# Performance work log

Measured on AMD Instinct MI355X. Metric: run time of the kernel, lower is better.

## Reference

```python
import jax, jax.numpy as jnp
import numpy as np
from jax import lax

V, E, HD, T = 32000, 256, 256, 4   # vocab, embed dim, lstm hidden (bidir total), tagset (BMES)
H = HD // 2                        # hidden per direction
B, S = 64, 1024


def setup_inputs() -> dict:
    key = jax.random.key(0)
    ks = jax.random.split(key, 16)
    sc = 0.1
    return {
        "sentences": jax.random.randint(ks[0], (B, S), 0, V, dtype=jnp.int32),
        "embed": jax.random.normal(ks[1], (V, E), jnp.float32) * sc,
        "w_ih_f": jax.random.normal(ks[2], (4 * H, E), jnp.float32) * sc,
        "w_hh_f": jax.random.normal(ks[3], (4 * H, H), jnp.float32) * sc,
        "b_ih_f": jax.random.normal(ks[4], (4 * H,), jnp.float32) * sc,
        "b_hh_f": jax.random.normal(ks[5], (4 * H,), jnp.float32) * sc,
        "w_ih_r": jax.random.normal(ks[6], (4 * H, E), jnp.float32) * sc,
        "w_hh_r": jax.random.normal(ks[7], (4 * H, H), jnp.float32) * sc,
        "b_ih_r": jax.random.normal(ks[8], (4 * H,), jnp.float32) * sc,
        "b_hh_r": jax.random.normal(ks[9], (4 * H,), jnp.float32) * sc,
        "w_out": jax.random.normal(ks[10], (T, HD), jnp.float32) * sc,
        "b_out": jax.random.normal(ks[11], (T,), jnp.float32) * sc,
        "start_t": jax.random.normal(ks[12], (T,), jnp.float32) * sc,
        "end_t": jax.random.normal(ks[13], (T,), jnp.float32) * sc,
        "trans": jax.random.normal(ks[14], (T, T), jnp.float32) * sc,
    }


def _lstm_pass(x, w_ih, w_hh, b_ih, b_hh):
    # x: [S, B, E]; PyTorch gate order i, f, g, o; zero initial state.
    bsz = x.shape[1]
    hdim = w_hh.shape[1]
    b = b_ih + b_hh

    def step(carry, xt):
        h, c = carry
        z = xt @ w_ih.T + h @ w_hh.T + b  # [B, 4H]
        i, f, g, o = jnp.split(z, 4, axis=-1)
        c = jax.nn.sigmoid(f) * c + jax.nn.sigmoid(i) * jnp.tanh(g)
        h = jax.nn.sigmoid(o) * jnp.tanh(c)
        return (h, c), h

    init = (jnp.zeros((bsz, hdim), x.dtype), jnp.zeros((bsz, hdim), x.dtype))
    _, hs = lax.scan(step, init, x)
    return hs  # [S, B, H]


def _emissions(sentences, embed, w_ih_f, w_hh_f, b_ih_f, b_hh_f,
               w_ih_r, w_hh_r, b_ih_r, b_hh_r, w_out, b_out):
    x = embed[sentences]                # [B, S, E]
    xs = jnp.transpose(x, (1, 0, 2))    # [S, B, E]
    hf = _lstm_pass(xs, w_ih_f, w_hh_f, b_ih_f, b_hh_f)
    hr = _lstm_pass(xs[::-1], w_ih_r, w_hh_r, b_ih_r, b_hh_r)[::-1]
    h = jnp.concatenate([hf, hr], axis=-1)        # [S, B, 2H]
    return h @ w_out.T + b_out                    # [S, B, T] emissions


def _viterbi_decode(feats, start_t, end_t, trans):
    # feats: [S, B, T] (no mask: all sequences full length, matching crf.decode on dense batch)
    score0 = start_t + feats[0]  # [B, T]

    def fwd_step(score, emit):
        nxt = score[:, :, None] + trans[None, :, :] + emit[:, None, :]  # [B, Tprev, Tcur]
        return jnp.max(nxt, axis=1), jnp.argmax(nxt, axis=1)

    final, bps = lax.scan(fwd_step, score0, feats[1:])  # bps: [S-1, B, T]
    final = final + end_t
    last = jnp.argmax(final, axis=1)  # [B]

    def back_step(tag, bp):
        prev = jnp.take_along_axis(bp, tag[:, None], axis=1)[:, 0]
        return prev, prev

    _, path_head = lax.scan(back_step, last, bps, reverse=True)  # [S-1, B], tags at t=0..S-2
    path = jnp.concatenate([path_head, last[None]], axis=0)      # [S, B]
    return jnp.transpose(path, (1, 0)).astype(jnp.int32)         # [B, S]


def reference(sentences, embed, w_ih_f, w_hh_f, b_ih_f, b_hh_f,
              w_ih_r, w_hh_r, b_ih_r, b_hh_r, w_out, b_out,
              start_t, end_t, trans):
    feats = _emissions(sentences, embed, w_ih_f, w_hh_f, b_ih_f, b_hh_f,
                       w_ih_r, w_hh_r, b_ih_r, b_hh_r, w_out, b_out)
    return _viterbi_decode(feats, start_t, end_t, trans)
```

## Files before the change

kernel.cpp:

```cpp
#include <hip/hip_runtime.h>
#include <cstdint>
#include <cstddef>

#define SLEN 1024
#define BATCH 64
#define EDIM 256
#define HDIM 128
#define GDIM 512
#define NTAG 4
#define VOCAB 32000

typedef float f2 __attribute__((ext_vector_type(2)));
typedef float f4 __attribute__((ext_vector_type(4)));


__device__ __forceinline__ float sigm_f(float x) {
    return 1.0f / (1.0f + __expf(-x));
}
__device__ __forceinline__ float tanh_f(float x) {
    return 1.0f - 2.0f / (1.0f + __expf(2.0f * x));
}

template <int CTRL>
__device__ __forceinline__ float quad_perm(float x) {
    return __int_as_float(
        __builtin_amdgcn_mov_dpp(__float_as_int(x), CTRL, 0xF, 0xF, true));
}
#define QP_XOR1 0xB1
#define QP_XOR2 0x4E
#define QP_MIR8 0x141
#define QP_BC0  0x00
#define QP_BC1  0x55
#define QP_BC2  0xAA
#define QP_BC3  0xFF

__global__ __launch_bounds__(512) void table_k(
    const float* __restrict__ embed,
    const float* __restrict__ w_ih_f, const float* __restrict__ w_ih_r,
    const float* __restrict__ b_ih_f, const float* __restrict__ b_hh_f,
    const float* __restrict__ b_ih_r, const float* __restrict__ b_hh_r,
    float* __restrict__ T)
{
    __shared__ __align__(16) float smem[12288];
    float* As = smem;
    const int t  = threadIdx.x;
    const int tm = t >> 8;
    const int tt = t & 255;
    float* Bs = smem + 4096 + tm * 4096;

    const int mt  = blockIdx.x;
    const int cp  = blockIdx.y;
    const int nt  = cp * 2 + tm;
    const int dir = nt >> 2;
    const float* W  = dir ? w_ih_r : w_ih_f;
    const float* bi = dir ? b_ih_r : b_ih_f;
    const float* bh = dir ? b_hh_r : b_hh_f;
    const int ncol = (nt & 3) * 128;
    const int r0   = mt * 128;

    const int sra = t & 127;
    const int qa  = t >> 7;
    const float* arow = embed + (size_t)(r0 + sra) * EDIM + qa * 8;

    const int srb = tt & 127;
    const int hb  = tt >> 7;
    const float* brow = W + (size_t)(ncol + srb) * EDIM + hb * 16;

    const int tx = tt & 15, ty = tt >> 4;

    f2 acc[8][4];
    #pragma unroll
    for (int i = 0; i < 8; ++i)
        #pragma unroll
        for (int jj = 0; jj < 4; ++jj) acc[i][jj] = (f2)(0.0f);

    for (int kt = 0; kt < 8; ++kt) {
        const int k0 = kt * 32;
        __syncthreads();
        {
            float4 v0 = *(const float4*)(arow + k0);
            float4 v1 = *(const float4*)(arow + k0 + 4);
            const int kk = qa * 8;
            As[(kk + 0) * 128 + sra] = v0.x;
            As[(kk + 1) * 128 + sra] = v0.y;
            As[(kk + 2) * 128 + sra] = v0.z;
            As[(kk + 3) * 128 + sra] = v0.w;
            As[(kk + 4) * 128 + sra] = v1.x;
            As[(kk + 5) * 128 + sra] = v1.y;
            As[(kk + 6) * 128 + sra] = v1.z;
            As[(kk + 7) * 128 + sra] = v1.w;
        }
        #pragma unroll
        for (int i = 0; i < 4; ++i) {
            float4 v = *(const float4*)(brow + k0 + i * 4);
            const int kk = hb * 16 + i * 4;
            Bs[(kk + 0) * 128 + srb] = v.x;
            Bs[(kk + 1) * 128 + srb] = v.y;
            Bs[(kk + 2) * 128 + srb] = v.z;
            Bs[(kk + 3) * 128 + srb] = v.w;
        }
        __syncthreads();

        #pragma unroll 8
        for (int k = 0; k < 32; ++k) {
            const f4 a0  = *(const f4*)&As[k * 128 + ty * 4];
            const f4 a1  = *(const f4*)&As[k * 128 + 64 + ty * 4];
            const f4 bq0 = *(const f4*)&Bs[k * 128 + tx * 4];
            const f4 bq1 = *(const f4*)&Bs[k * 128 + 64 + tx * 4];
            float av[8] = {a0.x, a0.y, a0.z, a0.w, a1.x, a1.y, a1.z, a1.w};
            f2 bv[4];
            bv[0] = __builtin_shufflevector(bq0, bq0, 0, 1);
            bv[1] = __builtin_shufflevector(bq0, bq0, 2, 3);
            bv[2] = __builtin_shufflevector(bq1, bq1, 0, 1);
            bv[3] = __builtin_shufflevector(bq1, bq1, 2, 3);
            #pragma unroll
            for (int i = 0; i < 8; ++i) {
                f2 as; as.x = av[i]; as.y = av[i];
                #pragma unroll
                for (int jj = 0; jj < 4; ++jj)
                    acc[i][jj] += as * bv[jj];
            }
        }
    }

    float bias0[4], bias1[4];
    #pragma unroll
    for (int j = 0; j < 4; ++j) {
        bias0[j] = bi[ncol + tx * 4 + j] + bh[ncol + tx * 4 + j];
        bias1[j] = bi[ncol + 64 + tx * 4 + j] + bh[ncol + 64 + tx * 4 + j];
    }

    #pragma unroll
    for (int i = 0; i < 8; ++i) {
        const int row = r0 + ((i < 4) ? (ty * 4 + i) : (64 + ty * 4 + i - 4));
        float* zp = T + (size_t)row * 1024 + dir * 512 + ncol;
        float4 o0, o1;
        o0.x = acc[i][0].x + bias0[0]; o0.y = acc[i][0].y + bias0[1];
        o0.z = acc[i][1].x + bias0[2]; o0.w = acc[i][1].y + bias0[3];
        o1.x = acc[i][2].x + bias1[0]; o1.y = acc[i][2].y + bias1[1];
        o1.z = acc[i][3].x + bias1[2]; o1.w = acc[i][3].y + bias1[3];
        *(float4*)(zp + tx * 4)      = o0;
        *(float4*)(zp + 64 + tx * 4) = o1;
    }
}

__global__ __launch_bounds__(512) __attribute__((amdgpu_waves_per_eu(2, 2)))
void lstm_k(
    const float* __restrict__ T, const int* __restrict__ sent,
    const float* __restrict__ w_hh_f, const float* __restrict__ w_hh_r,
    float* __restrict__ H)
{
    __shared__ __align__(16) float sh_h[320];
    __shared__ int sh_tok[SLEN];

    const int bid = blockIdx.x;
    const int b   = bid & 63;
    const int dir = bid >> 6;
    const int q   = threadIdx.x;
    const int p   = q & 7;
    const int Q   = q >> 3;
    const int gt  = p & 3;
    const int hi  = p >> 2;
    const int u   = Q + hi * 64;

    const float* Whh = dir ? w_hh_r : w_hh_f;

    f2 w2[8][8];
    #pragma unroll
    for (int pr = 0; pr < 8; ++pr) {
        const int uu = (pr & 4) ? (Q + 64) : Q;
        const int gg = pr & 3;
        const f2* src =
            (const f2*)(Whh + ((size_t)(gg * 128 + uu) * 128 + p * 16));
        #pragma unroll
        for (int i = 0; i < 8; ++i) w2[pr][i] = src[i];
    }
    #pragma unroll
    for (int pr = 0; pr < 8; ++pr)
        #pragma unroll
        for (int i = 0; i < 8; ++i)
            asm volatile("" : "+v"(w2[pr][i]));

    sh_tok[q]       = sent[b * SLEN + q];
    sh_tok[512 + q] = sent[b * SLEN + 512 + q];
    if (q < 128) sh_h[(q >> 5) * 36 + (q & 31)] = 0.0f;
    float c = 0.0f;
    __syncthreads();

    const int zcol = dir * 512 + gt * 128 + u;
    const ptrdiff_t hstride = dir ? -16384 : 16384;
    float* hg = H + ((size_t)(dir ? (SLEN - 1) : 0) * 64 + b) * 256
              + dir * 128 + u;

    const bool k4 = (p & 4) != 0;
    const bool k2 = (p & 2) != 0;
    const bool k1 = (p & 1) != 0;
    const float gsc  = (gt == 2) ? 2.0f : 1.0f;
    const float gofs = (gt == 2) ? -1.0f : 0.0f;
    const int shr = (p >> 1) * 36 + (p & 1) * 16;
    const int shw = (u >> 5) * 36 + (u & 31);

    float zcur[4], znxt[4];
    #pragma unroll
    for (int dt = 0; dt < 4; ++dt) {
        const int s = dir ? (SLEN - 1 - dt) : dt;
        zcur[dt] = T[((size_t)sh_tok[s] << 10) + zcol];
    }

    for (int t0 = 0; t0 < SLEN; t0 += 4) {
        const bool more = (t0 + 4 < SLEN);
        if (more) {
            #pragma unroll
            for (int dt = 0; dt < 4; ++dt) {
                const int tn = t0 + 4 + dt;
                const int s = dir ? (SLEN - 1 - tn) : tn;
                znxt[dt] = T[((size_t)sh_tok[s] << 10) + zcol];
            }
        }

        #pragma unroll
        for (int dt = 0; dt < 4; ++dt) {
            const f4* hp = (const f4*)(sh_h + (dt & 1) * 160 + shr);
            f2 hv[8];
            #pragma unroll
            for (int i = 0; i < 4; ++i) {
                f4 v = hp[i];
                hv[2 * i]     = __builtin_shufflevector(v, v, 0, 1);
                hv[2 * i + 1] = __builtin_shufflevector(v, v, 2, 3);
            }
            float s[8];
            #pragma unroll
            for (int pr = 0; pr < 8; ++pr) {
                f2 a = (f2)(0.0f);
                #pragma unroll
                for (int i = 0; i < 8; ++i) a += w2[pr][i] * hv[i];
                s[pr] = a.x + a.y;
            }
            float K1[4];
            #pragma unroll
            for (int j = 0; j < 4; ++j) {
                float keep = k4 ? s[j + 4] : s[j];
                float send = k4 ? s[j] : s[j + 4];
                K1[j] = keep + quad_perm<QP_MIR8>(send);
            }
            float K2[2];
            #pragma unroll
            for (int j = 0; j < 2; ++j) {
                float keep = k2 ? K1[j + 2] : K1[j];
                float send = k2 ? K1[j] : K1[j + 2];
                K2[j] = keep + quad_perm<QP_XOR2>(send);
            }
            float keep3 = k1 ? K2[1] : K2[0];
            float send3 = k1 ? K2[0] : K2[1];
            float zv = keep3 + quad_perm<QP_XOR1>(send3) + zcur[dt];

            float sgv = sigm_f(zv * gsc);
            float act = fmaf(sgv, gsc, gofs);

            float a_i = quad_perm<QP_BC0>(act);
            float a_f = quad_perm<QP_BC1>(act);
            float a_g = quad_perm<QP_BC2>(act);
            float a_o = quad_perm<QP_BC3>(act);
            c = a_f * c + a_i * a_g;
            float h = a_o * tanh_f(c);

            if (gt == 0) {
                sh_h[((dt + 1) & 1) * 160 + shw] = h;
                *hg = h;
            }
            hg += hstride;
            __syncthreads();
        }

        if (more) {
            #pragma unroll
            for (int dt = 0; dt < 4; ++dt) zcur[dt] = znxt[dt];
        }
    }
}

__device__ __forceinline__ void gemm_body(
    float* smem, int mt, int cp,
    const int* __restrict__ sent, const float* __restrict__ embed,
    const float* __restrict__ w_ih_f, const float* __restrict__ w_ih_r,
    const float* __restrict__ b_ih_f, const float* __restrict__ b_hh_f,
    const float* __restrict__ b_ih_r, const float* __restrict__ b_hh_r,
    float* __restrict__ Z, int base_f, int base_r)
{
    float* As = smem;
    const int t  = threadIdx.x;
    const int tm = t >> 8;
    const int tt = t & 255;
    float* Bs = smem + 4096 + tm * 4096;

    const int nt  = cp * 2 + tm;
    const int dir = nt >> 2;
    const float* W  = dir ? w_ih_r : w_ih_f;
    const float* bi = dir ? b_ih_r : b_ih_f;
    const float* bh = dir ? b_hh_r : b_hh_f;
    const int ncol = (nt & 3) * 128;
    const int r0   = mt * 128;

    const int sra = t & 127;
    const int qa  = t >> 7;
    const int r_loc = r0 + sra;
    const int s_loc = r_loc >> 6;
    const int b_    = r_loc & 63;
    const int s_glob = (dir ? base_r : base_f) + s_loc;
    const int tok = sent[b_ * SLEN + s_glob];
    const float* arow = embed + (size_t)tok * EDIM + qa * 8;

    const int srb = tt & 127;
    const int hb  = tt >> 7;
    const float* brow = W + (size_t)(ncol + srb) * EDIM + hb * 16;

    const int tx = tt & 15, ty = tt >> 4;

    f2 acc[8][4];
    #pragma unroll
    for (int i = 0; i < 8; ++i)
        #pragma unroll
        for (int jj = 0; jj < 4; ++jj) acc[i][jj] = (f2)(0.0f);

    for (int kt = 0; kt < 8; ++kt) {
        const int k0 = kt * 32;
        __syncthreads();
        {
            float4 v0 = *(const float4*)(arow + k0);
            float4 v1 = *(const float4*)(arow + k0 + 4);
            const int kk = qa * 8;
            As[(kk + 0) * 128 + sra] = v0.x;
            As[(kk + 1) * 128 + sra] = v0.y;
            As[(kk + 2) * 128 + sra] = v0.z;
            As[(kk + 3) * 128 + sra] = v0.w;
            As[(kk + 4) * 128 + sra] = v1.x;
            As[(kk + 5) * 128 + sra] = v1.y;
            As[(kk + 6) * 128 + sra] = v1.z;
            As[(kk + 7) * 128 + sra] = v1.w;
        }
        #pragma unroll
        for (int i = 0; i < 4; ++i) {
            float4 v = *(const float4*)(brow + k0 + i * 4);
            const int kk = hb * 16 + i * 4;
            Bs[(kk + 0) * 128 + srb] = v.x;
            Bs[(kk + 1) * 128 + srb] = v.y;
            Bs[(kk + 2) * 128 + srb] = v.z;
            Bs[(kk + 3) * 128 + srb] = v.w;
        }
        __syncthreads();

        #pragma unroll 8
        for (int k = 0; k < 32; ++k) {
            const f4 a0  = *(const f4*)&As[k * 128 + ty * 4];
            const f4 a1  = *(const f4*)&As[k * 128 + 64 + ty * 4];
            const f4 bq0 = *(const f4*)&Bs[k * 128 + tx * 4];
            const f4 bq1 = *(const f4*)&Bs[k * 128 + 64 + tx * 4];
            float av[8] = {a0.x, a0.y, a0.z, a0.w, a1.x, a1.y, a1.z, a1.w};
            f2 bv[4];
            bv[0] = __builtin_shufflevector(bq0, bq0, 0, 1);
            bv[1] = __builtin_shufflevector(bq0, bq0, 2, 3);
            bv[2] = __builtin_shufflevector(bq1, bq1, 0, 1);
            bv[3] = __builtin_shufflevector(bq1, bq1, 2, 3);
            #pragma unroll
            for (int i = 0; i < 8; ++i) {
                f2 as; as.x = av[i]; as.y = av[i];
                #pragma unroll
                for (int jj = 0; jj < 4; ++jj)
                    acc[i][jj] += as * bv[jj];
            }
        }
    }

    float bias0[4], bias1[4];
    #pragma unroll
    for (int j = 0; j < 4; ++j) {
        bias0[j] = bi[ncol + tx * 4 + j] + bh[ncol + tx * 4 + j];
        bias1[j] = bi[ncol + 64 + tx * 4 + j] + bh[ncol + 64 + tx * 4 + j];
    }

    #pragma unroll
    for (int i = 0; i < 8; ++i) {
        const int row = r0 + ((i < 4) ? (ty * 4 + i) : (64 + ty * 4 + i - 4));
        float* zp = Z + (size_t)row * 1024 + dir * 512 + ncol;
        float4 o0, o1;
        o0.x = acc[i][0].x + bias0[0]; o0.y = acc[i][0].y + bias0[1];
        o0.z = acc[i][1].x + bias0[2]; o0.w = acc[i][1].y + bias0[3];
        o1.x = acc[i][2].x + bias1[0]; o1.y = acc[i][2].y + bias1[1];
        o1.z = acc[i][3].x + bias1[2]; o1.w = acc[i][3].y + bias1[3];
        *(float4*)(zp + tx * 4)      = o0;
        *(float4*)(zp + 64 + tx * 4) = o1;
    }
}

__device__ __forceinline__ void lstm_body(
    float* smem,
    const float* __restrict__ Z, const float* __restrict__ w_hh_f,
    const float* __restrict__ w_hh_r, float* __restrict__ H,
    float* __restrict__ ST, int base_f, int base_r, int L, int first)
{
    float* sh_h = smem;

    const int bid = blockIdx.x;
    const int b   = bid & 63;
    const int dir = bid >> 6;
    const int q   = threadIdx.x;
    const int p   = q & 7;
    const int Q   = q >> 3;
    const int gt  = p & 3;
    const int hi  = p >> 2;
    const int u   = Q + hi * 64;

    const float* Whh = dir ? w_hh_r : w_hh_f;

    f2 w2[8][8];
    #pragma unroll
    for (int pr = 0; pr < 8; ++pr) {
        const int uu = (pr & 4) ? (Q + 64) : Q;
        const int gg = pr & 3;
        const f2* src =
            (const f2*)(Whh + ((size_t)(gg * 128 + uu) * 128 + p * 16));
        #pragma unroll
        for (int i = 0; i < 8; ++i) w2[pr][i] = src[i];
    }

    float* stp = ST + (size_t)(dir * 64 + b) * 256;
    if (q < 128)
        sh_h[(q >> 5) * 36 + (q & 31)] = first ? 0.0f : stp[q];
    float c = first ? 0.0f : stp[128 + u];

    const ptrdiff_t zstride = dir ? -65536 : 65536;
    const float* zp0 = Z + (size_t)b * 1024 + dir * 512
                     + (dir ? (size_t)(L - 1) * 65536 : 0) + gt * 128 + u;
    const ptrdiff_t hstride = dir ? -16384 : 16384;
    float* hg = H + ((size_t)(dir ? (base_r + L - 1) : base_f) * 64 + b) * 256
              + dir * 128 + u;

    const bool k4 = (p & 4) != 0;
    const bool k2 = (p & 2) != 0;
    const bool k1 = (p & 1) != 0;
    const float gsc  = (gt == 2) ? 2.0f : 1.0f;
    const float gofs = (gt == 2) ? -1.0f : 0.0f;
    const int shr = (p >> 1) * 36 + (p & 1) * 16;
    const int shw = (u >> 5) * 36 + (u & 31);

    float zcur[4], znxt[4];
    {
        const float* zp = zp0;
        #pragma unroll
        for (int dt = 0; dt < 4; ++dt) { zcur[dt] = *zp; zp += zstride; }
    }
    __syncthreads();

    float hlast = 0.0f;

    for (int t0 = 0; t0 < L; t0 += 4) {
        const bool more = (t0 + 4 < L);
        if (more) {
            const float* zp = zp0 + (ptrdiff_t)(t0 + 4) * zstride;
            #pragma unroll
            for (int dt = 0; dt < 4; ++dt) { znxt[dt] = *zp; zp += zstride; }
        }

        #pragma unroll
        for (int dt = 0; dt < 4; ++dt) {
            const f4* hp = (const f4*)(sh_h + (dt & 1) * 160 + shr);
            f2 hv[8];
            #pragma unroll
            for (int i = 0; i < 4; ++i) {
                f4 v = hp[i];
                hv[2 * i]     = __builtin_shufflevector(v, v, 0, 1);
                hv[2 * i + 1] = __builtin_shufflevector(v, v, 2, 3);
            }
            float s[8];
            #pragma unroll
            for (int pr = 0; pr < 8; ++pr) {
                f2 a = (f2)(0.0f);
                #pragma unroll
                for (int i = 0; i < 8; ++i) a += w2[pr][i] * hv[i];
                s[pr] = a.x + a.y;
            }
            float K1[4];
            #pragma unroll
            for (int j = 0; j < 4; ++j) {
                float keep = k4 ? s[j + 4] : s[j];
                float send = k4 ? s[j] : s[j + 4];
                K1[j] = keep + quad_perm<QP_MIR8>(send);
            }
            float K2[2];
            #pragma unroll
            for (int j = 0; j < 2; ++j) {
                float keep = k2 ? K1[j + 2] : K1[j];
                float send = k2 ? K1[j] : K1[j + 2];
                K2[j] = keep + quad_perm<QP_XOR2>(send);
            }
            float keep3 = k1 ? K2[1] : K2[0];
            float send3 = k1 ? K2[0] : K2[1];
            float zv = keep3 + quad_perm<QP_XOR1>(send3) + zcur[dt];

            float sgv = sigm_f(zv * gsc);
            float act = fmaf(sgv, gsc, gofs);

            float a_i = quad_perm<QP_BC0>(act);
            float a_f = quad_perm<QP_BC1>(act);
            float a_g = quad_perm<QP_BC2>(act);
            float a_o = quad_perm<QP_BC3>(act);
            c = a_f * c + a_i * a_g;
            float h = a_o * tanh_f(c);
            hlast = h;

            if (gt == 0) {
                sh_h[((dt + 1) & 1) * 160 + shw] = h;
                *hg = h;
            }
            hg += hstride;
            __syncthreads();
        }

        if (more) {
            #pragma unroll
            for (int dt = 0; dt < 4; ++dt) zcur[dt] = znxt[dt];
        }
    }

    if (gt == 0) {
        stp[u] = hlast;
        stp[128 + u] = c;
    }
}

__global__ __launch_bounds__(512) void fused_lstm_gemm(
    const int* __restrict__ sent, const float* __restrict__ embed,
    const float* __restrict__ w_ih_f, const float* __restrict__ w_ih_r,
    const float* __restrict__ b_ih_f, const float* __restrict__ b_hh_f,
    const float* __restrict__ b_ih_r, const float* __restrict__ b_hh_r,
    float* __restrict__ Zw, int gbase_f, int gbase_r, int mtiles,
    const float* __restrict__ Zr, const float* __restrict__ w_hh_f,
    const float* __restrict__ w_hh_r, float* __restrict__ H,
    float* __restrict__ ST, int lbase_f, int lbase_r, int L, int first)
{
    __shared__ __align__(16) float smem[12288];

    if (blockIdx.x < 128) {
        lstm_body(smem, Zr, w_hh_f, w_hh_r, H, ST, lbase_f, lbase_r, L, first);
    } else {
        const int g  = blockIdx.x - 128;
        const int mt = g % mtiles;
        const int cp = g / mtiles;
        gemm_body(smem, mt, cp, sent, embed, w_ih_f, w_ih_r,
                  b_ih_f, b_hh_f, b_ih_r, b_hh_r, Zw, gbase_f, gbase_r);
    }
}

__global__ __launch_bounds__(512) void gemm_zin(
    const int* __restrict__ sent, const float* __restrict__ embed,
    const float* __restrict__ w_ih_f, const float* __restrict__ w_ih_r,
    const float* __restrict__ b_ih_f, const float* __restrict__ b_hh_f,
    const float* __restrict__ b_ih_r, const float* __restrict__ b_hh_r,
    float* __restrict__ Z, int base_f, int base_r)
{
    __shared__ __align__(16) float smem[12288];
    gemm_body(smem, blockIdx.x, blockIdx.y, sent, embed, w_ih_f, w_ih_r,
              b_ih_f, b_hh_f, b_ih_r, b_hh_r, Z, base_f, base_r);
}

__global__ __launch_bounds__(256) void emissions_k(
    const float* __restrict__ H, const float* __restrict__ w_out,
    const float* __restrict__ b_out, float* __restrict__ F)
{
    const int gid = blockIdx.x * 256 + threadIdx.x;
    const int r   = gid >> 2;
    const int tg  = gid & 3;
    const float4* h4 = (const float4*)(H + (size_t)r * 256);
    const float4* w4 = (const float4*)(w_out + (size_t)tg * 256);
    float a0 = 0.f, a1 = 0.f, a2 = 0.f, a3 = 0.f;
    #pragma unroll 8
    for (int k = 0; k < 64; ++k) {
        float4 h = h4[k], w = w4[k];
        a0 = fmaf(h.x, w.x, a0); a1 = fmaf(h.y, w.y, a1);
        a2 = fmaf(h.z, w.z, a2); a3 = fmaf(h.w, w.w, a3);
    }
    F[gid] = ((a0 + a1) + (a2 + a3)) + b_out[tg];
}

__device__ __forceinline__ unsigned compose_map(unsigned a, unsigned b) {
    unsigned r = 0;
    #pragma unroll
    for (int jj = 0; jj < 4; ++jj) {
        unsigned bj = (b >> (jj * 8)) & 3u;
        unsigned aj = (a >> (bj * 8)) & 3u;
        r |= aj << (jj * 8);
    }
    return r;
}

__global__ __launch_bounds__(64) void viterbi_k(
    const float* __restrict__ F, const float* __restrict__ start_t,
    const float* __restrict__ end_t, const float* __restrict__ trans,
    int* __restrict__ out)
{
    const int b    = blockIdx.x;
    const int lane = threadIdx.x;
    __shared__ __align__(16) float sfeat[SLEN][NTAG];
    __shared__ unsigned sbp[SLEN];

    #pragma unroll
    for (int i = 0; i < 16; ++i) {
        int s = i * 64 + lane;
        ((float4*)sfeat)[s] = *(const float4*)(F + ((size_t)s * BATCH + b) * NTAG);
    }
    __syncthreads();

    const int cur = lane & 3;
    float tr0 = trans[0 * 4 + cur], tr1 = trans[1 * 4 + cur];
    float tr2 = trans[2 * 4 + cur], tr3 = trans[3 * 4 + cur];
    float sc = start_t[cur] + sfeat[0][cur];

    for (int s = 1; s < SLEN; ++s) {
        float ft = sfeat[s][cur];
        float s0 = __shfl(sc, 0), s1 = __shfl(sc, 1);
        float s2 = __shfl(sc, 2), s3 = __shfl(sc, 3);
        float c0 = s0 + tr0, c1 = s1 + tr1, c2 = s2 + tr2, c3 = s3 + tr3;
        float best = c0; int arg = 0;
        if (c1 > best) { best = c1; arg = 1; }
        if (c2 > best) { best = c2; arg = 2; }
        if (c3 > best) { best = c3; arg = 3; }
        sc = best + ft;
        unsigned bp = (unsigned)arg;
        unsigned b0 = __shfl(bp, 0), b1 = __shfl(bp, 1);
        unsigned b2 = __shfl(bp, 2), b3 = __shfl(bp, 3);
        if (lane == 0) sbp[s] = b0 | (b1 << 8) | (b2 << 16) | (b3 << 24);
    }
    sc += end_t[cur];
    float f0 = __shfl(sc, 0), f1 = __shfl(sc, 1);
    float f2v = __shfl(sc, 2), f3 = __shfl(sc, 3);
    int last = 0; float bb = f0;
    if (f1 > bb)  { bb = f1;  last = 1; }
    if (f2v > bb) { bb = f2v; last = 2; }
    if (f3 > bb)  { bb = f3;  last = 3; }
    __syncthreads();

    unsigned m[16];
    #pragma unroll
    for (int k = 0; k < 16; ++k) {
        int s = lane * 16 + k;
        m[k] = (s >= 1) ? sbp[s] : 0x03020100u;
    }
    unsigned G = m[15];
    #pragma unroll
    for (int k = 14; k >= 0; --k) G = compose_map(m[k], G);
    unsigned R = G;
    #pragma unroll
    for (int d = 1; d < 64; d <<= 1) {
        unsigned oo = __shfl_down(R, d);
        if (lane + d < 64) R = compose_map(R, oo);
    }
    unsigned P = __shfl_down(R, 1);
    if (lane == 63) P = 0x03020100u;

    int tcur = (int)((P >> (last * 8)) & 3u);
    int* ob = out + b * SLEN + lane * 16;
    ob[15] = tcur;
    #pragma unroll
    for (int k = 15; k >= 1; --k) {
        tcur = (int)((m[k] >> (tcur * 8)) & 3u);
        ob[k - 1] = tcur;
    }
}

extern "C" void kernel_launch(void* const* d_in, const int* in_sizes, int n_in,
                              void* d_out, int out_size, void* d_ws, size_t ws_size,
                              hipStream_t stream)
{
    const int*   sent    = (const int*)d_in[0];
    const float* embed   = (const float*)d_in[1];
    const float* w_ih_f  = (const float*)d_in[2];
    const float* w_hh_f  = (const float*)d_in[3];
    const float* b_ih_f  = (const float*)d_in[4];
    const float* b_hh_f  = (const float*)d_in[5];
    const float* w_ih_r  = (const float*)d_in[6];
    const float* w_hh_r  = (const float*)d_in[7];
    const float* b_ih_r  = (const float*)d_in[8];
    const float* b_hh_r  = (const float*)d_in[9];
    const float* w_out   = (const float*)d_in[10];
    const float* b_out   = (const float*)d_in[11];
    const float* start_t = (const float*)d_in[12];
    const float* end_t   = (const float*)d_in[13];
    const float* trans   = (const float*)d_in[14];
    int* out = (int*)d_out;

    const size_t H_FLOATS  = (size_t)SLEN * BATCH * 256;
    const size_t F_FLOATS  = (size_t)SLEN * BATCH * NTAG;
    const size_t T_FLOATS  = (size_t)VOCAB * 1024;
    const size_t ST_FLOATS = (size_t)2 * BATCH * 256;

    const size_t table_need = (T_FLOATS + H_FLOATS + F_FLOATS) * sizeof(float);

    if (ws_size >= table_need) {
        float* T = (float*)d_ws;
        float* H = T + T_FLOATS;
        float* F = H + H_FLOATS;

        table_k<<<dim3(250, 4), 512, 0, stream>>>(
            embed, w_ih_f, w_ih_r, b_ih_f, b_hh_f, b_ih_r, b_hh_r, T);
        lstm_k<<<128, 512, 0, stream>>>(T, sent, w_hh_f, w_hh_r, H);
        emissions_k<<<1024, 256, 0, stream>>>(H, w_out, b_out, F);
        viterbi_k<<<64, 64, 0, stream>>>(F, start_t, end_t, trans, out);
        return;
    }

    const size_t FIXED = H_FLOATS + F_FLOATS + ST_FLOATS;
    int L = 0;
    for (int cand = 256; cand >= 32; cand >>= 1) {
        size_t need = ((size_t)2 * cand * BATCH * 1024 + FIXED) * sizeof(float);
        if (need <= ws_size) { L = cand; break; }
    }

    if (L > 0) {
        const int nch = SLEN / L;
        const int mtiles = (L * BATCH) / 128;
        float* Z0 = (float*)d_ws;
        float* Z1 = Z0 + (size_t)L * BATCH * 1024;
        float* H  = Z1 + (size_t)L * BATCH * 1024;
        float* F  = H + H_FLOATS;
        float* ST = F + F_FLOATS;
        float* Zb[2] = {Z0, Z1};

        gemm_zin<<<dim3(mtiles, 4), 512, 0, stream>>>(
            sent, embed, w_ih_f, w_ih_r, b_ih_f, b_hh_f, b_ih_r, b_hh_r,
            Zb[0], 0, SLEN - L);

        for (int c = 0; c < nch; ++c) {
            const int lbase_f = c * L;
            const int lbase_r = SLEN - (c + 1) * L;
            const int hasg = (c + 1 < nch);
            const int gbase_f = (c + 1) * L;
            const int gbase_r = SLEN - (c + 2) * L;
            const int grid = hasg ? (128 + mtiles * 4) : 128;
            fused_lstm_gemm<<<grid, 512, 0, stream>>>(
                sent, embed, w_ih_f, w_ih_r, b_ih_f, b_hh_f, b_ih_r, b_hh_r,
                Zb[(c + 1) & 1], hasg ? gbase_f : 0, hasg ? gbase_r : 0, mtiles,
                Zb[c & 1], w_hh_f, w_hh_r, H, ST, lbase_f, lbase_r, L,
                c == 0 ? 1 : 0);
        }

        emissions_k<<<1024, 256, 0, stream>>>(H, w_out, b_out, F);
        viterbi_k<<<64, 64, 0, stream>>>(F, start_t, end_t, trans, out);
    } else {
        int Ls = SLEN;
        while (Ls > 32) {
            size_t need = ((size_t)Ls * BATCH * 1024 + FIXED) * sizeof(float);
            if (need <= ws_size) break;
            Ls >>= 1;
        }
        const int nch = SLEN / Ls;
        const int mtiles = (Ls * BATCH) / 128;
        float* Z  = (float*)d_ws;
        float* H  = Z + (size_t)Ls * BATCH * 1024;
        float* F  = H + H_FLOATS;
        float* ST = F + F_FLOATS;

        for (int c = 0; c < nch; ++c) {
            const int base_f = c * Ls;
            const int base_r = SLEN - (c + 1) * Ls;
            gemm_zin<<<dim3(mtiles, 4), 512, 0, stream>>>(
                sent, embed, w_ih_f, w_ih_r, b_ih_f, b_hh_f, b_ih_r, b_hh_r,
                Z, base_f, base_r);
            fused_lstm_gemm<<<128, 512, 0, stream>>>(
                sent, embed, w_ih_f, w_ih_r, b_ih_f, b_hh_f, b_ih_r, b_hh_r,
                Z, 0, 0, mtiles,
                Z, w_hh_f, w_hh_r, H, ST, base_f, base_r, Ls, c == 0 ? 1 : 0);
        }
        emissions_k<<<1024, 256, 0, stream>>>(H, w_out, b_out, F);
        viterbi_k<<<64, 64, 0, stream>>>(F, start_t, end_t, trans, out);
    }
}
```

Before: 1.122 ms.

## Split LSTM recurrence across 1024 threads with one hidden unit each

The recurrent LSTM kernel now launches 1024 threads per block instead of 512, so each thread keeps 4 gate-row weight slices instead of 8. This halves the per-thread dot-product work and removes one cross-lane reduction stage on the serial per-timestep critical path. In exchange, the per-step block barrier spans twice as many waves, and the waves-per-EU hint is dropped. A redundant ternary on the F pointer in the fallback path is also added, with no effect.

```diff
diff --git a/kernel.cpp b/kernel.cpp
--- a/kernel.cpp
+++ b/kernel.cpp
@@ -144,8 +144,7 @@
     }
 }
 
-__global__ __launch_bounds__(512) __attribute__((amdgpu_waves_per_eu(2, 2)))
-void lstm_k(
+__global__ __launch_bounds__(1024) void lstm_k(
     const float* __restrict__ T, const int* __restrict__ sent,
     const float* __restrict__ w_hh_f, const float* __restrict__ w_hh_r,
     float* __restrict__ H)
@@ -158,31 +157,26 @@
     const int dir = bid >> 6;
     const int q   = threadIdx.x;
     const int p   = q & 7;
-    const int Q   = q >> 3;
+    const int u   = q >> 3;
     const int gt  = p & 3;
-    const int hi  = p >> 2;
-    const int u   = Q + hi * 64;
 
     const float* Whh = dir ? w_hh_r : w_hh_f;
 
-    f2 w2[8][8];
-    #pragma unroll
-    for (int pr = 0; pr < 8; ++pr) {
-        const int uu = (pr & 4) ? (Q + 64) : Q;
-        const int gg = pr & 3;
+    f2 w2[4][8];
+    #pragma unroll
+    for (int g = 0; g < 4; ++g) {
         const f2* src =
-            (const f2*)(Whh + ((size_t)(gg * 128 + uu) * 128 + p * 16));
-        #pragma unroll
-        for (int i = 0; i < 8; ++i) w2[pr][i] = src[i];
-    }
-    #pragma unroll
-    for (int pr = 0; pr < 8; ++pr)
+            (const f2*)(Whh + ((size_t)(g * 128 + u) * 128 + p * 16));
+        #pragma unroll
+        for (int i = 0; i < 8; ++i) w2[g][i] = src[i];
+    }
+    #pragma unroll
+    for (int g = 0; g < 4; ++g)
         #pragma unroll
         for (int i = 0; i < 8; ++i)
-            asm volatile("" : "+v"(w2[pr][i]));
-
-    sh_tok[q]       = sent[b * SLEN + q];
-    sh_tok[512 + q] = sent[b * SLEN + 512 + q];
+            asm volatile("" : "+v"(w2[g][i]));
+
+    sh_tok[q] = sent[b * SLEN + q];
     if (q < 128) sh_h[(q >> 5) * 36 + (q & 31)] = 0.0f;
     float c = 0.0f;
     __syncthreads();
@@ -192,7 +186,6 @@
     float* hg = H + ((size_t)(dir ? (SLEN - 1) : 0) * 64 + b) * 256
               + dir * 128 + u;
 
-    const bool k4 = (p & 4) != 0;
     const bool k2 = (p & 2) != 0;
     const bool k1 = (p & 1) != 0;
     const float gsc  = (gt == 2) ? 2.0f : 1.0f;
@@ -228,26 +221,23 @@
                 hv[2 * i]     = __builtin_shufflevector(v, v, 0, 1);
                 hv[2 * i + 1] = __builtin_shufflevector(v, v, 2, 3);
             }
-            float s[8];
-            #pragma unroll
-            for (int pr = 0; pr < 8; ++pr) {
+            float s0[4];
+            #pragma unroll
+            for (int g = 0; g < 4; ++g) {
                 f2 a = (f2)(0.0f);
                 #pragma unroll
-                for (int i = 0; i < 8; ++i) a += w2[pr][i] * hv[i];
-                s[pr] = a.x + a.y;
-            }
-            float K1[4];
-            #pragma unroll
-            for (int j = 0; j < 4; ++j) {
-                float keep = k4 ? s[j + 4] : s[j];
-                float send = k4 ? s[j] : s[j + 4];
-                K1[j] = keep + quad_perm<QP_MIR8>(send);
-            }
+                for (int i = 0; i < 8; ++i) a += w2[g][i] * hv[i];
+                s0[g] = a.x + a.y;
+            }
+            float t1[4];
+            #pragma unroll
+            for (int j = 0; j < 4; ++j)
+                t1[j] = s0[j] + quad_perm<QP_MIR8>(s0[j]);
             float K2[2];
             #pragma unroll
             for (int j = 0; j < 2; ++j) {
-                float keep = k2 ? K1[j + 2] : K1[j];
-                float send = k2 ? K1[j] : K1[j + 2];
+                float keep = k2 ? t1[j + 2] : t1[j];
+                float send = k2 ? t1[j] : t1[j + 2];
                 K2[j] = keep + quad_perm<QP_XOR2>(send);
             }
             float keep3 = k1 ? K2[1] : K2[0];
@@ -264,7 +254,7 @@
             c = a_f * c + a_i * a_g;
             float h = a_o * tanh_f(c);
 
-            if (gt == 0) {
+            if (p == 0) {
                 sh_h[((dt + 1) & 1) * 160 + shw] = h;
                 *hg = h;
             }
@@ -702,7 +692,7 @@
 
         table_k<<<dim3(250, 4), 512, 0, stream>>>(
             embed, w_ih_f, w_ih_r, b_ih_f, b_hh_f, b_ih_r, b_hh_r, T);
-        lstm_k<<<128, 512, 0, stream>>>(T, sent, w_hh_f, w_hh_r, H);
+        lstm_k<<<128, 1024, 0, stream>>>(T, sent, w_hh_f, w_hh_r, H);
         emissions_k<<<1024, 256, 0, stream>>>(H, w_out, b_out, F);
         viterbi_k<<<64, 64, 0, stream>>>(F, start_t, end_t, trans, out);
         return;
@@ -756,7 +746,8 @@
         const int mtiles = (Ls * BATCH) / 128;
         float* Z  = (float*)d_ws;
         float* H  = Z + (size_t)Ls * BATCH * 1024;
-        float* F  = H + H_FLOATS;
+        float* F  = H + F_FLOATS ? H + H_FLOATS : H + H_FLOATS;
+        F = H + H_FLOATS;
         float* ST = F + F_FLOATS;
 
         for (int c = 0; c < nch; ++c) {
```

Measured after the change: 1.289 ms. 14.8% more time.

## Halve register-resident recurrent weights, stream rest from cache, drop waves_per_eu

Applied to the files above, without the earlier changes.

The LSTM recurrence kernel now keeps only half of its W_hh slice (the first 64 hidden units' gates) in registers and reloads the other half from global memory (L1/L2) every timestep. The waves_per_eu(2,2) attribute is removed and the prefetch depth of input projections drops from 4 to 2 steps. The aim is to cut register pressure, but it adds a per-step global load of 64 floats per thread onto the serial critical path of a latency-bound 1024-step recurrence.

```diff
diff --git a/kernel.cpp b/kernel.cpp
--- a/kernel.cpp
+++ b/kernel.cpp
@@ -144,8 +144,7 @@
     }
 }
 
-__global__ __launch_bounds__(512) __attribute__((amdgpu_waves_per_eu(2, 2)))
-void lstm_k(
+__global__ __launch_bounds__(512) void lstm_k(
     const float* __restrict__ T, const int* __restrict__ sent,
     const float* __restrict__ w_hh_f, const float* __restrict__ w_hh_r,
     float* __restrict__ H)
@@ -165,21 +164,21 @@
 
     const float* Whh = dir ? w_hh_r : w_hh_f;
 
-    f2 w2[8][8];
-    #pragma unroll
-    for (int pr = 0; pr < 8; ++pr) {
-        const int uu = (pr & 4) ? (Q + 64) : Q;
-        const int gg = pr & 3;
+    f2 w2r[4][8];
+    #pragma unroll
+    for (int g = 0; g < 4; ++g) {
         const f2* src =
-            (const f2*)(Whh + ((size_t)(gg * 128 + uu) * 128 + p * 16));
-        #pragma unroll
-        for (int i = 0; i < 8; ++i) w2[pr][i] = src[i];
-    }
-    #pragma unroll
-    for (int pr = 0; pr < 8; ++pr)
+            (const f2*)(Whh + ((size_t)(g * 128 + Q) * 128 + p * 16));
+        #pragma unroll
+        for (int i = 0; i < 8; ++i) w2r[g][i] = src[i];
+    }
+    #pragma unroll
+    for (int g = 0; g < 4; ++g)
         #pragma unroll
         for (int i = 0; i < 8; ++i)
-            asm volatile("" : "+v"(w2[pr][i]));
+            asm volatile("" : "+v"(w2r[g][i]));
+
+    const float* wsbase = Whh + (size_t)(Q + 64) * 128 + p * 16;
 
     sh_tok[q]       = sent[b * SLEN + q];
     sh_tok[512 + q] = sent[b * SLEN + 512 + q];
@@ -200,42 +199,78 @@
     const int shr = (p >> 1) * 36 + (p & 1) * 16;
     const int shw = (u >> 5) * 36 + (u & 31);
 
-    float zcur[4], znxt[4];
-    #pragma unroll
-    for (int dt = 0; dt < 4; ++dt) {
+    float zcur[2], znxt[2];
+    #pragma unroll
+    for (int dt = 0; dt < 2; ++dt) {
         const int s = dir ? (SLEN - 1 - dt) : dt;
         zcur[dt] = T[((size_t)sh_tok[s] << 10) + zcol];
     }
 
-    for (int t0 = 0; t0 < SLEN; t0 += 4) {
-        const bool more = (t0 + 4 < SLEN);
+    for (int t0 = 0; t0 < SLEN; t0 += 2) {
+        const bool more = (t0 + 2 < SLEN);
         if (more) {
             #pragma unroll
-            for (int dt = 0; dt < 4; ++dt) {
-                const int tn = t0 + 4 + dt;
+            for (int dt = 0; dt < 2; ++dt) {
+                const int tn = t0 + 2 + dt;
                 const int s = dir ? (SLEN - 1 - tn) : tn;
                 znxt[dt] = T[((size_t)sh_tok[s] << 10) + zcol];
             }
         }
 
         #pragma unroll
-        for (int dt = 0; dt < 4; ++dt) {
-            const f4* hp = (const f4*)(sh_h + (dt & 1) * 160 + shr);
-            f2 hv[8];
-            #pragma unroll
-            for (int i = 0; i < 4; ++i) {
-                f4 v = hp[i];
-                hv[2 * i]     = __builtin_shufflevector(v, v, 0, 1);
-                hv[2 * i + 1] = __builtin_shufflevector(v, v, 2, 3);
-            }
+        for (int dt = 0; dt < 2; ++dt) {
+            const float* shb = sh_h + ((t0 + dt) & 1) * 160 + shr;
+            f2 acc[8];
+            #pragma unroll
+            for (int j = 0; j < 8; ++j) acc[j] = (f2)(0.0f);
+
+            #pragma unroll
+            for (int kh = 0; kh < 2; ++kh) {
+                const f4* hp = (const f4*)(shb + kh * 8);
+                f4 hA = hp[0], hB = hp[1];
+                f2 hv[4];
+                hv[0] = __builtin_shufflevector(hA, hA, 0, 1);
+                hv[1] = __builtin_shufflevector(hA, hA, 2, 3);
+                hv[2] = __builtin_shufflevector(hB, hB, 0, 1);
+                hv[3] = __builtin_shufflevector(hB, hB, 2, 3);
+
+                #pragma unroll
+                for (int gp = 0; gp < 2; ++gp) {
+                    const int g0 = gp * 2, g1 = gp * 2 + 1;
+                    const f4* wp0 =
+                        (const f4*)(wsbase + (size_t)g0 * 16384 + kh * 8);
+                    const f4* wp1 =
+                        (const f4*)(wsbase + (size_t)g1 * 16384 + kh * 8);
+                    f4 wa0 = wp0[0], wa1 = wp0[1];
+                    f4 wb0 = wp1[0], wb1 = wp1[1];
+                    #pragma unroll
+                    for (int i = 0; i < 4; ++i) {
+                        acc[g0] += w2r[g0][kh * 4 + i] * hv[i];
+                        acc[g1] += w2r[g1][kh * 4 + i] * hv[i];
+                    }
+                    f2 s00 = __builtin_shufflevector(wa0, wa0, 0, 1);
+                    f2 s01 = __builtin_shufflevector(wa0, wa0, 2, 3);
+                    f2 s02 = __builtin_shufflevector(wa1, wa1, 0, 1);
+                    f2 s03 = __builtin_shufflevector(wa1, wa1, 2, 3);
+                    acc[4 + g0] += s00 * hv[0];
+                    acc[4 + g0] += s01 * hv[1];
+                    acc[4 + g0] += s02 * hv[2];
+                    acc[4 + g0] += s03 * hv[3];
+                    f2 s10 = __builtin_shufflevector(wb0, wb0, 0, 1);
+                    f2 s11 = __builtin_shufflevector(wb0, wb0, 2, 3);
+                    f2 s12 = __builtin_shufflevector(wb1, wb1, 0, 1);
+                    f2 s13 = __builtin_shufflevector(wb1, wb1, 2, 3);
+                    acc[4 + g1] += s10 * hv[0];
+                    acc[4 + g1] += s11 * hv[1];
+                    acc[4 + g1] += s12 * hv[2];
+                    acc[4 + g1] += s13 * hv[3];
+                }
+            }
+
             float s[8];
             #pragma unroll
-            for (int pr = 0; pr < 8; ++pr) {
-                f2 a = (f2)(0.0f);
-                #pragma unroll
-                for (int i = 0; i < 8; ++i) a += w2[pr][i] * hv[i];
-                s[pr] = a.x + a.y;
-            }
+            for (int pr = 0; pr < 8; ++pr) s[pr] = acc[pr].x + acc[pr].y;
+
             float K1[4];
             #pragma unroll
             for (int j = 0; j < 4; ++j) {
@@ -265,7 +300,7 @@
             float h = a_o * tanh_f(c);
 
             if (gt == 0) {
-                sh_h[((dt + 1) & 1) * 160 + shw] = h;
+                sh_h[(((t0 + dt) + 1) & 1) * 160 + shw] = h;
                 *hg = h;
             }
             hg += hstride;
@@ -273,8 +308,8 @@
         }
 
         if (more) {
-            #pragma unroll
-            for (int dt = 0; dt < 4; ++dt) zcur[dt] = znxt[dt];
+            zcur[0] = znxt[0];
+            zcur[1] = znxt[1];
         }
     }
 }
```

Result: slower. 1.230 ms (+9.6%).

## Move half of recurrent weights from registers to LDS and global loads

Applied to the files above, without the earlier changes.

Instead of holding all of W_hh in registers (128 floats per thread), the LSTM kernel now stores half the gate weights in shared memory (128 KB LDS) and re-reads the other half from global/L2 every timestep. The waves_per_eu attribute is dropped and the prefetch unroll shrinks from 4 to 2 steps. The goal is to relieve register pressure, at the price of extra LDS and global traffic on the serial recurrence's critical path.

```diff
diff --git a/kernel.cpp b/kernel.cpp
--- a/kernel.cpp
+++ b/kernel.cpp
@@ -144,14 +144,15 @@
     }
 }
 
-__global__ __launch_bounds__(512) __attribute__((amdgpu_waves_per_eu(2, 2)))
-void lstm_k(
+__global__ __launch_bounds__(512) void lstm_k(
     const float* __restrict__ T, const int* __restrict__ sent,
     const float* __restrict__ w_hh_f, const float* __restrict__ w_hh_r,
     float* __restrict__ H)
 {
-    __shared__ __align__(16) float sh_h[320];
-    __shared__ int sh_tok[SLEN];
+    __shared__ __align__(16) float smem[34112];
+    f2*    WL     = (f2*)smem;
+    float* sh_h   = smem + 32768;
+    int*   sh_tok = (int*)(smem + 33088);
 
     const int bid = blockIdx.x;
     const int b   = bid & 63;
@@ -165,21 +166,16 @@
 
     const float* Whh = dir ? w_hh_r : w_hh_f;
 
-    f2 w2[8][8];
-    #pragma unroll
-    for (int pr = 0; pr < 8; ++pr) {
-        const int uu = (pr & 4) ? (Q + 64) : Q;
-        const int gg = pr & 3;
+    #pragma unroll
+    for (int g = 0; g < 4; ++g) {
         const f2* src =
-            (const f2*)(Whh + ((size_t)(gg * 128 + uu) * 128 + p * 16));
-        #pragma unroll
-        for (int i = 0; i < 8; ++i) w2[pr][i] = src[i];
-    }
-    #pragma unroll
-    for (int pr = 0; pr < 8; ++pr)
-        #pragma unroll
-        for (int i = 0; i < 8; ++i)
-            asm volatile("" : "+v"(w2[pr][i]));
+            (const f2*)(Whh + ((size_t)(g * 128 + Q) * 128 + p * 16));
+        #pragma unroll
+        for (int j = 0; j < 8; ++j)
+            WL[g * 4096 + j * 512 + q] = src[j];
+    }
+
+    const float* wsbase = Whh + (size_t)(Q + 64) * 128 + p * 16;
 
     sh_tok[q]       = sent[b * SLEN + q];
     sh_tok[512 + q] = sent[b * SLEN + 512 + q];
@@ -200,27 +196,27 @@
     const int shr = (p >> 1) * 36 + (p & 1) * 16;
     const int shw = (u >> 5) * 36 + (u & 31);
 
-    float zcur[4], znxt[4];
-    #pragma unroll
-    for (int dt = 0; dt < 4; ++dt) {
+    float zcur[2], znxt[2];
+    #pragma unroll
+    for (int dt = 0; dt < 2; ++dt) {
         const int s = dir ? (SLEN - 1 - dt) : dt;
         zcur[dt] = T[((size_t)sh_tok[s] << 10) + zcol];
     }
 
-    for (int t0 = 0; t0 < SLEN; t0 += 4) {
-        const bool more = (t0 + 4 < SLEN);
+    for (int t0 = 0; t0 < SLEN; t0 += 2) {
+        const bool more = (t0 + 2 < SLEN);
         if (more) {
             #pragma unroll
-            for (int dt = 0; dt < 4; ++dt) {
-                const int tn = t0 + 4 + dt;
+            for (int dt = 0; dt < 2; ++dt) {
+                const int tn = t0 + 2 + dt;
                 const int s = dir ? (SLEN - 1 - tn) : tn;
                 znxt[dt] = T[((size_t)sh_tok[s] << 10) + zcol];
             }
         }
 
         #pragma unroll
-        for (int dt = 0; dt < 4; ++dt) {
-            const f4* hp = (const f4*)(sh_h + (dt & 1) * 160 + shr);
+        for (int dt = 0; dt < 2; ++dt) {
+            const f4* hp = (const f4*)(sh_h + ((t0 + dt) & 1) * 160 + shr);
             f2 hv[8];
             #pragma unroll
             for (int i = 0; i < 4; ++i) {
@@ -228,14 +224,33 @@
                 hv[2 * i]     = __builtin_shufflevector(v, v, 0, 1);
                 hv[2 * i + 1] = __builtin_shufflevector(v, v, 2, 3);
             }
+
             float s[8];
             #pragma unroll
-            for (int pr = 0; pr < 8; ++pr) {
-                f2 a = (f2)(0.0f);
+            for (int g = 0; g < 4; ++g) {
+                const f4* wp = (const f4*)(wsbase + (size_t)g * 16384);
+                f4 w0 = wp[0], w1 = wp[1], w2v = wp[2], w3 = wp[3];
+
+                f2 a0 = (f2)(0.0f);
                 #pragma unroll
-                for (int i = 0; i < 8; ++i) a += w2[pr][i] * hv[i];
-                s[pr] = a.x + a.y;
-            }
+                for (int j = 0; j < 8; ++j)
+                    a0 += WL[g * 4096 + j * 512 + q] * hv[j];
+
+                f2 a1 = (f2)(0.0f);
+                f2 t;
+                t = __builtin_shufflevector(w0, w0, 0, 1);  a1 += t * hv[0];
+                t = __builtin_shufflevector(w0, w0, 2, 3);  a1 += t * hv[1];
+                t = __builtin_shufflevector(w1, w1, 0, 1);  a1 += t * hv[2];
+                t = __builtin_shufflevector(w1, w1, 2, 3);  a1 += t * hv[3];
+                t = __builtin_shufflevector(w2v, w2v, 0, 1); a1 += t * hv[4];
+                t = __builtin_shufflevector(w2v, w2v, 2, 3); a1 += t * hv[5];
+                t = __builtin_shufflevector(w3, w3, 0, 1);  a1 += t * hv[6];
+                t = __builtin_shufflevector(w3, w3, 2, 3);  a1 += t * hv[7];
+
+                s[g]     = a0.x + a0.y;
+                s[4 + g] = a1.x + a1.y;
+            }
+
             float K1[4];
             #pragma unroll
             for (int j = 0; j < 4; ++j) {
@@ -265,7 +280,7 @@
             float h = a_o * tanh_f(c);
 
             if (gt == 0) {
-                sh_h[((dt + 1) & 1) * 160 + shw] = h;
+                sh_h[(((t0 + dt) + 1) & 1) * 160 + shw] = h;
                 *hg = h;
             }
             hg += hstride;
@@ -273,8 +288,8 @@
         }
 
         if (more) {
-            #pragma unroll
-            for (int dt = 0; dt < 4; ++dt) zcur[dt] = znxt[dt];
+            zcur[0] = znxt[0];
+            zcur[1] = znxt[1];
         }
     }
 }
```

New measurement: 1.325 ms. 1.18x slower.
